# Optimization experiments

Measured on AMD Instinct MI355X. Metric: run time of the kernel, lower is better.

## Reference

```python
import jax, jax.numpy as jnp
import numpy as np

IMG = 224          # mask height/width, hardcoded in the module
OUT = 256          # Linear(224*224 -> 256)
BOX = 20           # half-width of the square mask around the farthest joint


def setup_inputs() -> dict:
    key = jax.random.key(0)
    k1, k2, k3, k4 = jax.random.split(key, 4)
    B, J, T = 256, 25, 64
    rgbfuture = jax.random.normal(k1, (B, OUT), dtype=jnp.float32)
    # normalized joint coords kept in [0.1, 0.9] so pixel_x in [22, 201] (original
    # code has no x-clamping and would hit numpy negative-slice wraparound otherwise)
    skeleton_future = 0.1 + 0.8 * jax.random.uniform(k2, (B, J, T, 3), dtype=jnp.float32)
    W = jax.random.normal(k3, (OUT, IMG * IMG), dtype=jnp.float32) / np.sqrt(IMG * IMG)
    b = jax.random.normal(k4, (OUT,), dtype=jnp.float32) * 0.01
    return {"rgbfuture": rgbfuture, "skeleton_future": skeleton_future, "W": W, "b": b}


def reference(rgbfuture, skeleton_future, W, b):
    B, J, T, _ = skeleton_future.shape
    mid = J // 2

    # distance of every joint trajectory to the middle joint, per frame: [B, J, T]
    diff = skeleton_future - skeleton_future[:, mid:mid + 1]
    dist = jnp.linalg.norm(diff, axis=-1)
    t_max = jnp.argmax(dist, axis=-1)                       # [B, J]

    # farthest-frame coordinates per joint: [B, J, 3]
    pts = jnp.take_along_axis(skeleton_future, t_max[:, :, None, None], axis=2)[:, :, 0, :]
    px = (pts[..., 0] * IMG).astype(jnp.int32)              # int() truncation == floor (positive)
    py = (pts[..., 1] * IMG).astype(jnp.int32)

    rows = jnp.arange(IMG)
    # x-range: [px-20, px+20) (inputs guarantee in-frame)
    xm = (rows >= (px - BOX)[..., None]) & (rows < (px + BOX)[..., None])   # [B, J, IMG]
    # y-range with the module's explicit edge handling
    y_lo = jnp.where(py < BOX, 0, py - BOX)
    y_hi = jnp.where(py > IMG - BOX, IMG, py + BOX)
    ym = (rows >= y_lo[..., None]) & (rows < y_hi[..., None])               # [B, J, IMG]

    keep = jnp.arange(J) != mid                              # middle joint is skipped
    box = xm[:, :, :, None] & ym[:, :, None, :] & keep[None, :, None, None]  # [B, J, IMG, IMG]
    mask = jnp.any(box, axis=1).astype(rgbfuture.dtype)      # torch.max over joints == union

    merged = mask.reshape(B, IMG * IMG) @ W.T + b            # [B, 256]
    return rgbfuture * merged
```

## Files before the change

kernel.cpp:

```cpp
#include <hip/hip_runtime.h>
#include <hip/hip_bf16.h>
#include <stdint.h>

#define IMG   224
#define OUTD  256
#define BATCH 256
#define JD    25
#define TD    64
#define MIDJ  12
#define BOXR  20

#define OFF_RUNS 25804800u
#define OFF_PART 33144832u
#define OFF_CNT  35241984u


__global__ void KA(const float* __restrict__ W, __hip_bfloat16* __restrict__ P,
                   const float* __restrict__ skel, uint32_t* __restrict__ runs,
                   uint8_t* __restrict__ cnt) {
    const int id  = blockIdx.x;
    const int tid = threadIdx.x;

    __shared__ float lds[32][225];
    __shared__ float carry[8][32];
    __shared__ int s_px[JD], s_ylo[JD], s_yhi[JD];

    if (id < 1792) {
        const int xcd = id & 7;
        const int g   = id >> 3;
        const int oc  = g & 7;
        const int xi  = g >> 3;
        const int x   = xcd * 28 + xi;
        const int o0  = oc * 32;

        #pragma unroll
        for (int it = 0; it < 28; ++it) {
            const int k = it * 256 + tid;
            const int r = k / 224;
            const int y = k - r * 224;
            lds[r][y] = __builtin_nontemporal_load(
                &W[(size_t)(o0 + r) * (IMG * IMG) + (size_t)x * IMG + y]);
        }
        __syncthreads();

        const int ol  = tid & 31;
        const int seg = tid >> 5;
        const int y0  = seg * 28;

        float ssum = 0.0f;
        #pragma unroll
        for (int i = 0; i < 28; ++i) ssum += lds[ol][y0 + i];
        carry[seg][ol] = ssum;
        __syncthreads();

        float s = 0.0f;
        for (int s2 = 0; s2 < seg; ++s2) s += carry[s2][ol];

        __hip_bfloat16* p = P + ((size_t)x * 225) * 256 + o0 + ol;
        if (seg == 0) p[0] = __float2bfloat16(0.0f);
        #pragma unroll
        for (int i = 0; i < 28; ++i) {
            s += lds[ol][y0 + i];
            p[(size_t)(y0 + i + 1) * 256] = __float2bfloat16(s);
        }
        return;
    }

    const int b = id - 1792;
    const int wave = tid >> 6;
    const int t = tid & 63;

    const float* sb = skel + (size_t)b * JD * TD * 3;
    const float mx = sb[(MIDJ * TD + t) * 3 + 0];
    const float my = sb[(MIDJ * TD + t) * 3 + 1];
    const float mz = sb[(MIDJ * TD + t) * 3 + 2];

    for (int j = wave; j < JD; j += 4) {
        const float ax = sb[(j * TD + t) * 3 + 0];
        const float ay = sb[(j * TD + t) * 3 + 1];
        const float az = sb[(j * TD + t) * 3 + 2];
        const float dx = ax - mx, dy = ay - my, dz = az - mz;
        const float d2 = __fadd_rn(__fadd_rn(__fmul_rn(dx, dx), __fmul_rn(dy, dy)),
                                   __fmul_rn(dz, dz));
        float bd = sqrtf(d2);
        int   bi = t;
        #pragma unroll
        for (int off = 1; off < 64; off <<= 1) {
            const float od = __shfl_xor(bd, off);
            const int   oi = __shfl_xor(bi, off);
            if (od > bd || (od == bd && oi < bi)) { bd = od; bi = oi; }
        }
        if (t == 0) {
            const float ptx = sb[(j * TD + bi) * 3 + 0];
            const float pty = sb[(j * TD + bi) * 3 + 1];
            const int px = (int)(ptx * 224.0f);
            const int py = (int)(pty * 224.0f);
            s_px[j]  = px;
            s_ylo[j] = (py < BOXR) ? 0 : (py - BOXR);
            s_yhi[j] = (py > IMG - BOXR) ? IMG : (py + BOXR);
        }
    }
    __syncthreads();

    const int x = tid;
    if (x >= IMG) return;

    unsigned long long m0 = 0, m1 = 0, m2 = 0, m3 = 0;
    for (int j = 0; j < JD; ++j) {
        if (j == MIDJ) continue;
        const int px = s_px[j];
        if (x >= px - BOXR && x < px + BOXR) {
            const int lo = s_ylo[j], hi = s_yhi[j];
            auto setw = [&](unsigned long long& mw, int wbase) {
                int l = lo - wbase; int h = hi - wbase;
                l = l < 0 ? 0 : l; h = h > 64 ? 64 : h;
                if (l < h) {
                    unsigned long long msk =
                        (h - l == 64) ? ~0ull : ((((1ull << (h - l)) - 1ull)) << l);
                    mw |= msk;
                }
            };
            setw(m0, 0); setw(m1, 64); setw(m2, 128); setw(m3, 192);
        }
    }

    uint32_t* rb = runs + ((size_t)b * IMG + x) * 32;
    int n = 0, start = -1;
    auto scanw = [&](unsigned long long bits, int wbase) {
        int pos = 0;
        while (pos < 64) {
            if (start < 0) {
                const unsigned long long tt = bits >> pos;
                if (!tt) return;
                pos += __builtin_ctzll(tt);
                start = wbase + pos;
            } else {
                const unsigned long long tt = (~bits) >> pos;
                if (!tt) return;
                pos += __builtin_ctzll(tt);
                rb[n] = (uint32_t)start | ((uint32_t)(wbase + pos) << 8);
                ++n; start = -1;
            }
        }
    };
    scanw(m0, 0); scanw(m1, 64); scanw(m2, 128); scanw(m3, 192);
    if (start >= 0) { rb[n] = (uint32_t)start | (224u << 8); ++n; }
    cnt[(size_t)b * IMG + x] = (uint8_t)n;
}

__global__ void k_accum(const uint32_t* __restrict__ runs,
                        const uint8_t* __restrict__ cnt,
                        const uint32_t* __restrict__ P32,
                        float* __restrict__ part) {
    const int b = blockIdx.x >> 3;
    const int s = blockIdx.x & 7;
    const int tid = threadIdx.x;
    const int x0 = s * 28;

    __shared__ uint8_t  scnt[28];
    __shared__ uint16_t soff[29];
    __shared__ uint32_t slist[28 * 12];

    if (tid < 28) scnt[tid] = cnt[(size_t)b * IMG + x0 + tid];
    __syncthreads();
    if (tid == 0) {
        uint16_t acc = 0;
        #pragma unroll
        for (int i = 0; i < 28; ++i) { soff[i] = acc; acc += scnt[i]; }
        soff[28] = acc;
    }
    __syncthreads();

    for (int e = tid; e < 28 * 12; e += 128) {
        const int xl = e / 12;
        const int j  = e - xl * 12;
        if (j < (int)scnt[xl]) {
            const uint32_t raw = runs[((size_t)b * IMG + x0 + xl) * 32 + j];
            slist[soff[xl] + j] = raw | ((uint32_t)xl << 17);
        }
    }
    __syncthreads();

    const int total = soff[28];
    const uint32_t* Pbase = P32 + (size_t)x0 * 225 * 128 + tid;
    float a0 = 0.0f, a1 = 0.0f, b0 = 0.0f, b1 = 0.0f;
    int i = 0;
    for (; i + 2 <= total; i += 2) {
        const uint32_t e0 = slist[i];
        const uint32_t e1 = slist[i + 1];
        const uint32_t* px0 = Pbase + (size_t)(e0 >> 17) * (225 * 128);
        const uint32_t* px1 = Pbase + (size_t)(e1 >> 17) * (225 * 128);
        const uint32_t va0 = px0[(size_t)(e0 & 255u) * 128];
        const uint32_t vc0 = px0[(size_t)((e0 >> 8) & 511u) * 128];
        const uint32_t va1 = px1[(size_t)(e1 & 255u) * 128];
        const uint32_t vc1 = px1[(size_t)((e1 >> 8) & 511u) * 128];
        a0 += __uint_as_float(vc0 << 16) - __uint_as_float(va0 << 16);
        a1 += __uint_as_float(vc0 & 0xffff0000u) - __uint_as_float(va0 & 0xffff0000u);
        b0 += __uint_as_float(vc1 << 16) - __uint_as_float(va1 << 16);
        b1 += __uint_as_float(vc1 & 0xffff0000u) - __uint_as_float(va1 & 0xffff0000u);
    }
    if (i < total) {
        const uint32_t e0 = slist[i];
        const uint32_t* px0 = Pbase + (size_t)(e0 >> 17) * (225 * 128);
        const uint32_t va0 = px0[(size_t)(e0 & 255u) * 128];
        const uint32_t vc0 = px0[(size_t)((e0 >> 8) & 511u) * 128];
        a0 += __uint_as_float(vc0 << 16) - __uint_as_float(va0 << 16);
        a1 += __uint_as_float(vc0 & 0xffff0000u) - __uint_as_float(va0 & 0xffff0000u);
    }

    float* pp = part + (((size_t)b * 8 + s) * 256) + (size_t)tid * 2;
    pp[0] = a0 + b0;
    pp[1] = a1 + b1;
}

__global__ void k_final(const float* __restrict__ rgb, const float* __restrict__ bias,
                        const float* __restrict__ part, float* __restrict__ out) {
    const int idx = blockIdx.x * 256 + threadIdx.x;
    const int b = idx >> 8, o = idx & 255;
    float m = bias[o];
    #pragma unroll
    for (int s = 0; s < 8; ++s) m += part[(((size_t)b * 8 + s) * 256) + o];
    out[idx] = rgb[idx] * m;
}

extern "C" void kernel_launch(void* const* d_in, const int* in_sizes, int n_in,
                              void* d_out, int out_size, void* d_ws, size_t ws_size,
                              hipStream_t stream) {
    const float* rgb  = (const float*)d_in[0];
    const float* skel = (const float*)d_in[1];
    const float* W    = (const float*)d_in[2];
    const float* bias = (const float*)d_in[3];
    float* out = (float*)d_out;

    uint8_t* ws = (uint8_t*)d_ws;
    __hip_bfloat16* P = (__hip_bfloat16*)(ws);
    uint32_t* runs = (uint32_t*)(ws + OFF_RUNS);
    float* part = (float*)(ws + OFF_PART);
    uint8_t* cnt = (uint8_t*)(ws + OFF_CNT);

    KA<<<dim3(2048), dim3(256), 0, stream>>>(W, P, skel, runs, cnt);
    k_accum<<<dim3(BATCH * 8), dim3(128), 0, stream>>>(runs, cnt, (const uint32_t*)P, part);
    k_final<<<dim3(BATCH), dim3(256), 0, stream>>>(rgb, bias, part, out);
}
```

Before: 45.43 us.

## Build compacted per-slab run lists in KA and widen prefix-sum blocks

The prefix-sum blocks now use 512 threads, cover 64 outputs each, and read W with 128-bit nontemporal loads. The mask stage counts run starts with popcount, exclusive-scans the counts within each 28-column slab in LDS, and writes a packed event list plus a per-slab count. This lets k_accum load its list directly instead of rebuilding offsets from per-column counts. k_accum also unrolls its gather loop four-way for more loads in flight. The cost is higher LDS use per block (64x225 floats), which can lower occupancy, plus a serial per-thread scan over up to 27 columns.

```diff
diff --git a/kernel.cpp b/kernel.cpp
--- a/kernel.cpp
+++ b/kernel.cpp
@@ -10,41 +10,48 @@
 #define MIDJ  12
 #define BOXR  20
 
-#define OFF_RUNS 25804800u
-#define OFF_PART 33144832u
-#define OFF_CNT  35241984u
+typedef float vfloat4 __attribute__((ext_vector_type(4)));
+
+#define OFF_EV   25804800u
+#define OFF_EVC  27901952u
+#define OFF_PART 27910144u
 
 
 __global__ void KA(const float* __restrict__ W, __hip_bfloat16* __restrict__ P,
-                   const float* __restrict__ skel, uint32_t* __restrict__ runs,
-                   uint8_t* __restrict__ cnt) {
+                   const float* __restrict__ skel, uint32_t* __restrict__ evlist,
+                   uint32_t* __restrict__ evcnt) {
     const int id  = blockIdx.x;
     const int tid = threadIdx.x;
 
-    __shared__ float lds[32][225];
-    __shared__ float carry[8][32];
+    __shared__ float lds[64][225];
+    __shared__ float carry[8][64];
     __shared__ int s_px[JD], s_ylo[JD], s_yhi[JD];
-
-    if (id < 1792) {
+    __shared__ uint32_t s_n[IMG];
+
+    if (id < 896) {
         const int xcd = id & 7;
         const int g   = id >> 3;
-        const int oc  = g & 7;
-        const int xi  = g >> 3;
+        const int oc  = g & 3;
+        const int xi  = g >> 2;
         const int x   = xcd * 28 + xi;
-        const int o0  = oc * 32;
-
-        #pragma unroll
-        for (int it = 0; it < 28; ++it) {
-            const int k = it * 256 + tid;
-            const int r = k / 224;
-            const int y = k - r * 224;
-            lds[r][y] = __builtin_nontemporal_load(
-                &W[(size_t)(o0 + r) * (IMG * IMG) + (size_t)x * IMG + y]);
+        const int o0  = oc * 64;
+
+        #pragma unroll
+        for (int it = 0; it < 7; ++it) {
+            const int k = it * 512 + tid;
+            const int r = k / 56;
+            const int c = k - r * 56;
+            const vfloat4 v = __builtin_nontemporal_load(
+                (const vfloat4*)&W[(size_t)(o0 + r) * (IMG * IMG) + (size_t)x * IMG + c * 4]);
+            lds[r][c * 4 + 0] = v.x;
+            lds[r][c * 4 + 1] = v.y;
+            lds[r][c * 4 + 2] = v.z;
+            lds[r][c * 4 + 3] = v.w;
         }
         __syncthreads();
 
-        const int ol  = tid & 31;
-        const int seg = tid >> 5;
+        const int ol  = tid & 63;
+        const int seg = tid >> 6;
         const int y0  = seg * 28;
 
         float ssum = 0.0f;
@@ -66,7 +73,7 @@
         return;
     }
 
-    const int b = id - 1792;
+    const int b = id - 896;
     const int wave = tid >> 6;
     const int t = tid & 63;
 
@@ -75,7 +82,7 @@
     const float my = sb[(MIDJ * TD + t) * 3 + 1];
     const float mz = sb[(MIDJ * TD + t) * 3 + 2];
 
-    for (int j = wave; j < JD; j += 4) {
+    for (int j = wave; j < JD; j += 8) {
         const float ax = sb[(j * TD + t) * 3 + 0];
         const float ay = sb[(j * TD + t) * 3 + 1];
         const float az = sb[(j * TD + t) * 3 + 2];
@@ -103,29 +110,44 @@
     __syncthreads();
 
     const int x = tid;
+    unsigned long long m0 = 0, m1 = 0, m2 = 0, m3 = 0;
+    uint32_t n = 0;
+    if (x < IMG) {
+        for (int j = 0; j < JD; ++j) {
+            if (j == MIDJ) continue;
+            const int px = s_px[j];
+            if (x >= px - BOXR && x < px + BOXR) {
+                const int lo = s_ylo[j], hi = s_yhi[j];
+                auto setw = [&](unsigned long long& mw, int wbase) {
+                    int l = lo - wbase; int h = hi - wbase;
+                    l = l < 0 ? 0 : l; h = h > 64 ? 64 : h;
+                    if (l < h) {
+                        unsigned long long msk =
+                            (h - l == 64) ? ~0ull : ((((1ull << (h - l)) - 1ull)) << l);
+                        mw |= msk;
+                    }
+                };
+                setw(m0, 0); setw(m1, 64); setw(m2, 128); setw(m3, 192);
+            }
+        }
+        const unsigned long long e0 = m0 & ~(m0 << 1);
+        const unsigned long long e1 = m1 & ~((m1 << 1) | (m0 >> 63));
+        const unsigned long long e2 = m2 & ~((m2 << 1) | (m1 >> 63));
+        const unsigned long long e3 = m3 & ~((m3 << 1) | (m2 >> 63));
+        n = (uint32_t)(__popcll(e0) + __popcll(e1) + __popcll(e2) + __popcll(e3));
+        s_n[x] = n;
+    }
+    __syncthreads();
     if (x >= IMG) return;
 
-    unsigned long long m0 = 0, m1 = 0, m2 = 0, m3 = 0;
-    for (int j = 0; j < JD; ++j) {
-        if (j == MIDJ) continue;
-        const int px = s_px[j];
-        if (x >= px - BOXR && x < px + BOXR) {
-            const int lo = s_ylo[j], hi = s_yhi[j];
-            auto setw = [&](unsigned long long& mw, int wbase) {
-                int l = lo - wbase; int h = hi - wbase;
-                l = l < 0 ? 0 : l; h = h > 64 ? 64 : h;
-                if (l < h) {
-                    unsigned long long msk =
-                        (h - l == 64) ? ~0ull : ((((1ull << (h - l)) - 1ull)) << l);
-                    mw |= msk;
-                }
-            };
-            setw(m0, 0); setw(m1, 64); setw(m2, 128); setw(m3, 192);
-        }
-    }
-
-    uint32_t* rb = runs + ((size_t)b * IMG + x) * 32;
-    int n = 0, start = -1;
+    const int sl = x / 28;
+    const int xl = x - sl * 28;
+    uint32_t off = 0;
+    for (int i = sl * 28; i < x; ++i) off += s_n[i];
+    if (xl == 27) evcnt[(size_t)b * 8 + sl] = off + n;
+
+    uint32_t* evs = evlist + ((size_t)b * 8 + sl) * 256 + off;
+    int k = 0, start = -1;
     auto scanw = [&](unsigned long long bits, int wbase) {
         int pos = 0;
         while (pos < 64) {
@@ -138,79 +160,74 @@
                 const unsigned long long tt = (~bits) >> pos;
                 if (!tt) return;
                 pos += __builtin_ctzll(tt);
-                rb[n] = (uint32_t)start | ((uint32_t)(wbase + pos) << 8);
-                ++n; start = -1;
+                evs[k] = (uint32_t)xl | ((uint32_t)start << 5)
+                                      | ((uint32_t)(wbase + pos) << 13);
+                ++k; start = -1;
             }
         }
     };
     scanw(m0, 0); scanw(m1, 64); scanw(m2, 128); scanw(m3, 192);
-    if (start >= 0) { rb[n] = (uint32_t)start | (224u << 8); ++n; }
-    cnt[(size_t)b * IMG + x] = (uint8_t)n;
-}
-
-__global__ void k_accum(const uint32_t* __restrict__ runs,
-                        const uint8_t* __restrict__ cnt,
+    if (start >= 0) { evs[k] = (uint32_t)xl | ((uint32_t)start << 5) | (224u << 13); }
+}
+
+__global__ void k_accum(const uint32_t* __restrict__ evlist,
+                        const uint32_t* __restrict__ evcnt,
                         const uint32_t* __restrict__ P32,
                         float* __restrict__ part) {
-    const int b = blockIdx.x >> 3;
-    const int s = blockIdx.x & 7;
+    const int bs  = blockIdx.x;
+    const int s   = bs & 7;
     const int tid = threadIdx.x;
-    const int x0 = s * 28;
-
-    __shared__ uint8_t  scnt[28];
-    __shared__ uint16_t soff[29];
-    __shared__ uint32_t slist[28 * 12];
-
-    if (tid < 28) scnt[tid] = cnt[(size_t)b * IMG + x0 + tid];
+    const int x0  = s * 28;
+
+    __shared__ uint32_t slist[256];
+
+    const uint32_t cntv = evcnt[bs];
+    slist[tid]       = evlist[(size_t)bs * 256 + tid];
+    slist[128 + tid] = evlist[(size_t)bs * 256 + 128 + tid];
     __syncthreads();
-    if (tid == 0) {
-        uint16_t acc = 0;
-        #pragma unroll
-        for (int i = 0; i < 28; ++i) { soff[i] = acc; acc += scnt[i]; }
-        soff[28] = acc;
-    }
-    __syncthreads();
-
-    for (int e = tid; e < 28 * 12; e += 128) {
-        const int xl = e / 12;
-        const int j  = e - xl * 12;
-        if (j < (int)scnt[xl]) {
-            const uint32_t raw = runs[((size_t)b * IMG + x0 + xl) * 32 + j];
-            slist[soff[xl] + j] = raw | ((uint32_t)xl << 17);
-        }
-    }
-    __syncthreads();
-
-    const int total = soff[28];
-    const uint32_t* Pbase = P32 + (size_t)x0 * 225 * 128 + tid;
-    float a0 = 0.0f, a1 = 0.0f, b0 = 0.0f, b1 = 0.0f;
+
+    const int total = (int)cntv;
+    const uint32_t* Pbase = P32 + (size_t)x0 * (225 * 128) + tid;
+
+    float a0 = 0.f, a1 = 0.f, b0 = 0.f, b1 = 0.f;
+    float c0 = 0.f, c1 = 0.f, d0 = 0.f, d1 = 0.f;
     int i = 0;
-    for (; i + 2 <= total; i += 2) {
-        const uint32_t e0 = slist[i];
-        const uint32_t e1 = slist[i + 1];
-        const uint32_t* px0 = Pbase + (size_t)(e0 >> 17) * (225 * 128);
-        const uint32_t* px1 = Pbase + (size_t)(e1 >> 17) * (225 * 128);
-        const uint32_t va0 = px0[(size_t)(e0 & 255u) * 128];
-        const uint32_t vc0 = px0[(size_t)((e0 >> 8) & 511u) * 128];
-        const uint32_t va1 = px1[(size_t)(e1 & 255u) * 128];
-        const uint32_t vc1 = px1[(size_t)((e1 >> 8) & 511u) * 128];
+    for (; i + 4 <= total; i += 4) {
+        const uint32_t e0 = slist[i], e1 = slist[i + 1];
+        const uint32_t e2 = slist[i + 2], e3 = slist[i + 3];
+        const uint32_t* p0 = Pbase + (size_t)(e0 & 31u) * (225 * 128);
+        const uint32_t* p1 = Pbase + (size_t)(e1 & 31u) * (225 * 128);
+        const uint32_t* p2 = Pbase + (size_t)(e2 & 31u) * (225 * 128);
+        const uint32_t* p3 = Pbase + (size_t)(e3 & 31u) * (225 * 128);
+        const uint32_t va0 = p0[(size_t)((e0 >> 5) & 255u) * 128];
+        const uint32_t vc0 = p0[(size_t)((e0 >> 13) & 255u) * 128];
+        const uint32_t va1 = p1[(size_t)((e1 >> 5) & 255u) * 128];
+        const uint32_t vc1 = p1[(size_t)((e1 >> 13) & 255u) * 128];
+        const uint32_t va2 = p2[(size_t)((e2 >> 5) & 255u) * 128];
+        const uint32_t vc2 = p2[(size_t)((e2 >> 13) & 255u) * 128];
+        const uint32_t va3 = p3[(size_t)((e3 >> 5) & 255u) * 128];
+        const uint32_t vc3 = p3[(size_t)((e3 >> 13) & 255u) * 128];
         a0 += __uint_as_float(vc0 << 16) - __uint_as_float(va0 << 16);
         a1 += __uint_as_float(vc0 & 0xffff0000u) - __uint_as_float(va0 & 0xffff0000u);
         b0 += __uint_as_float(vc1 << 16) - __uint_as_float(va1 << 16);
         b1 += __uint_as_float(vc1 & 0xffff0000u) - __uint_as_float(va1 & 0xffff0000u);
-    }
-    if (i < total) {
+        c0 += __uint_as_float(vc2 << 16) - __uint_as_float(va2 << 16);
+        c1 += __uint_as_float(vc2 & 0xffff0000u) - __uint_as_float(va2 & 0xffff0000u);
+        d0 += __uint_as_float(vc3 << 16) - __uint_as_float(va3 << 16);
+        d1 += __uint_as_float(vc3 & 0xffff0000u) - __uint_as_float(va3 & 0xffff0000u);
+    }
+    for (; i < total; ++i) {
         const uint32_t e0 = slist[i];
-        const uint32_t* px0 = Pbase + (size_t)(e0 >> 17) * (225 * 128);
-        const uint32_t va0 = px0[(size_t)(e0 & 255u) * 128];
-        const uint32_t vc0 = px0[(size_t)((e0 >> 8) & 511u) * 128];
+        const uint32_t* p0 = Pbase + (size_t)(e0 & 31u) * (225 * 128);
+        const uint32_t va0 = p0[(size_t)((e0 >> 5) & 255u) * 128];
+        const uint32_t vc0 = p0[(size_t)((e0 >> 13) & 255u) * 128];
         a0 += __uint_as_float(vc0 << 16) - __uint_as_float(va0 << 16);
         a1 += __uint_as_float(vc0 & 0xffff0000u) - __uint_as_float(va0 & 0xffff0000u);
     }
 
-    float* pp = part + (((size_t)b * 8 + s) * 256) + (size_t)tid * 2;
-    pp[0] = a0 + b0;
-    pp[1] = a1 + b1;
+    float* pp = part + ((size_t)bs * 256) + (size_t)tid * 2;
+    pp[0] = (a0 + b0) + (c0 + d0);
+    pp[1] = (a1 + b1) + (c1 + d1);
 }
 
 __global__ void k_final(const float* __restrict__ rgb, const float* __restrict__ bias,
@@ -234,11 +251,11 @@
 
     uint8_t* ws = (uint8_t*)d_ws;
     __hip_bfloat16* P = (__hip_bfloat16*)(ws);
-    uint32_t* runs = (uint32_t*)(ws + OFF_RUNS);
+    uint32_t* evlist = (uint32_t*)(ws + OFF_EV);
+    uint32_t* evcnt  = (uint32_t*)(ws + OFF_EVC);
     float* part = (float*)(ws + OFF_PART);
-    uint8_t* cnt = (uint8_t*)(ws + OFF_CNT);
-
-    KA<<<dim3(2048), dim3(256), 0, stream>>>(W, P, skel, runs, cnt);
-    k_accum<<<dim3(BATCH * 8), dim3(128), 0, stream>>>(runs, cnt, (const uint32_t*)P, part);
+
+    KA<<<dim3(1152), dim3(512), 0, stream>>>(W, P, skel, evlist, evcnt);
+    k_accum<<<dim3(BATCH * 8), dim3(128), 0, stream>>>(evlist, evcnt, (const uint32_t*)P, part);
     k_final<<<dim3(BATCH), dim3(256), 0, stream>>>(rgb, bias, part, out);
 }
```

Result: faster. 41.76 us (-8.1%).
